# Kernel optimization log

Measured on AMD Instinct MI355X. Metric: run time of the kernel, lower is better.

## Reference

```python
import jax, jax.numpy as jnp
import numpy as np

DIM = 1024
HEADS = 16
HIDDEN = 4096
EPS = 1e-5

def setup_inputs() -> dict:
    key = jax.random.key(0)
    ks = jax.random.split(key, 8)
    s = 0.02
    return {
        "x": jax.random.normal(ks[0], (4, 1024, DIM), dtype=jnp.float32),
        "ln1_g": jnp.ones((DIM,), jnp.float32),
        "ln1_b": jnp.zeros((DIM,), jnp.float32),
        "w_qkv": jax.random.normal(ks[1], (DIM, 3 * DIM), jnp.float32) * s,
        "b_qkv": jnp.zeros((3 * DIM,), jnp.float32),
        "w_proj": jax.random.normal(ks[2], (DIM, DIM), jnp.float32) * s,
        "b_proj": jnp.zeros((DIM,), jnp.float32),
        "ln2_g": jnp.ones((DIM,), jnp.float32),
        "ln2_b": jnp.zeros((DIM,), jnp.float32),
        "w_fc1": jax.random.normal(ks[3], (DIM, HIDDEN), jnp.float32) * s,
        "b_fc1": jnp.zeros((HIDDEN,), jnp.float32),
        "w_fc2": jax.random.normal(ks[4], (HIDDEN, DIM), jnp.float32) * s,
        "b_fc2": jnp.zeros((DIM,), jnp.float32),
    }

def _layernorm(x, g, b):
    mu = jnp.mean(x, axis=-1, keepdims=True)
    var = jnp.mean(jnp.square(x - mu), axis=-1, keepdims=True)
    return (x - mu) * jax.lax.rsqrt(var + EPS) * g + b

def _block(x, ln1_g, ln1_b, w_qkv, b_qkv, w_proj, b_proj,
           ln2_g, ln2_b, w_fc1, b_fc1, w_fc2, b_fc2):
    B, N, C = x.shape
    H = HEADS
    Dh = C // H
    scale = Dh ** -0.5
    # --- attention branch (pre-norm) ---
    h = _layernorm(x, ln1_g, ln1_b)
    qkv = h @ w_qkv + b_qkv                       # [B,N,3C]
    qkv = qkv.reshape(B, N, 3, H, Dh)
    q, k, v = qkv[:, :, 0], qkv[:, :, 1], qkv[:, :, 2]  # [B,N,H,Dh]
    attn = jnp.einsum("bnhd,bmhd->bhnm", q, k) * scale  # [B,H,N,N]
    attn = jax.nn.softmax(attn, axis=-1)
    o = jnp.einsum("bhnm,bmhd->bnhd", attn, v).reshape(B, N, C)
    x = x + (o @ w_proj + b_proj)
    # --- MLP branch (pre-norm) ---
    h = _layernorm(x, ln2_g, ln2_b)
    h = jax.nn.gelu(h @ w_fc1 + b_fc1, approximate=False)
    x = x + (h @ w_fc2 + b_fc2)
    return x

def reference(x, ln1_g, ln1_b, w_qkv, b_qkv, w_proj, b_proj,
              ln2_g, ln2_b, w_fc1, b_fc1, w_fc2, b_fc2):
    return _block(x, ln1_g, ln1_b, w_qkv, b_qkv, w_proj, b_proj,
                  ln2_g, ln2_b, w_fc1, b_fc1, w_fc2, b_fc2)
```

## Files before the change

### kernel.cpp

```cpp
#include <hip/hip_runtime.h>
#include <hip/hip_bf16.h>

typedef __attribute__((ext_vector_type(8))) short bf16x8;
typedef __attribute__((ext_vector_type(4))) float f32x4;

__device__ __forceinline__ ushort f2bf(float f) {
  unsigned int u = __float_as_uint(f);
  u += 0x7fffu + ((u >> 16) & 1u);
  return (ushort)(u >> 16);
}

__device__ __forceinline__ void gl_lds16(const void* g, void* l) {
  __builtin_amdgcn_global_load_lds(
      (const __attribute__((address_space(1))) void*)g,
      (__attribute__((address_space(3))) void*)l, 16, 0, 0);
}

#define SB() __builtin_amdgcn_sched_barrier(0)

__global__ __launch_bounds__(256) void transpose_w(
    const float* __restrict__ W, ushort* __restrict__ Wt, int K, int N) {
  __shared__ float tile[32][33];
  const int tx = threadIdx.x, ty = threadIdx.y;
  const int bx = blockIdx.x, by = blockIdx.y;
#pragma unroll
  for (int j = 0; j < 4; j++)
    tile[ty + j * 8][tx] = W[(size_t)(by * 32 + ty + j * 8) * N + bx * 32 + tx];
  __syncthreads();
#pragma unroll
  for (int j = 0; j < 4; j++)
    Wt[(size_t)(bx * 32 + ty + j * 8) * K + by * 32 + tx] =
        f2bf(tile[tx][ty + j * 8]);
}

__global__ __launch_bounds__(256) void transpose_v(
    const ushort* __restrict__ qkv, ushort* __restrict__ vt) {
  __shared__ ushort tile[32][33];
  const int tx = threadIdx.x, ty = threadIdx.y;
  const int n0 = blockIdx.x * 32;
  const int d0 = blockIdx.y * 32;
  const int bh = blockIdx.z;
  const int bidx = bh >> 4, h = bh & 15;
#pragma unroll
  for (int j = 0; j < 4; j++)
    tile[ty + j * 8][tx] =
        qkv[(size_t)(bidx * 1024 + n0 + ty + j * 8) * 3072 + 2048 + h * 64 +
            d0 + tx];
  __syncthreads();
#pragma unroll
  for (int j = 0; j < 4; j++)
    vt[(size_t)(bh * 64 + d0 + ty + j * 8) * 1024 + n0 + tx] =
        tile[tx][ty + j * 8];
}

__global__ __launch_bounds__(256) void ln_bf16(
    const float* __restrict__ x, const float* __restrict__ g,
    const float* __restrict__ b, ushort* __restrict__ out) {
  const int row = blockIdx.x;
  const int t = threadIdx.x;
  float4 v = ((const float4*)(x + (size_t)row * 1024))[t];
  float s = v.x + v.y + v.z + v.w;
  float ss = v.x * v.x + v.y * v.y + v.z * v.z + v.w * v.w;
#pragma unroll
  for (int msk = 1; msk < 64; msk <<= 1) {
    s += __shfl_xor(s, msk);
    ss += __shfl_xor(ss, msk);
  }
  __shared__ float red[8];
  const int wv = t >> 6, ln = t & 63;
  if (ln == 0) { red[wv * 2] = s; red[wv * 2 + 1] = ss; }
  __syncthreads();
  s = red[0] + red[2] + red[4] + red[6];
  ss = red[1] + red[3] + red[5] + red[7];
  const float mu = s * (1.0f / 1024.0f);
  const float var = ss * (1.0f / 1024.0f) - mu * mu;
  const float rstd = rsqrtf(var + 1e-5f);
  float4 gv = ((const float4*)g)[t];
  float4 bv = ((const float4*)b)[t];
  ushort4 o;
  o.x = f2bf((v.x - mu) * rstd * gv.x + bv.x);
  o.y = f2bf((v.y - mu) * rstd * gv.y + bv.y);
  o.z = f2bf((v.z - mu) * rstd * gv.z + bv.z);
  o.w = f2bf((v.w - mu) * rstd * gv.w + bv.w);
  ((ushort4*)(out + (size_t)row * 1024))[t] = o;
}

template <int BM, int BN, int NW, int OCC, int EPI>
__global__ __launch_bounds__(NW * 64, OCC) void gemm32(
    const ushort* __restrict__ A, const ushort* __restrict__ Bt,
    const float* __restrict__ bias, const float* __restrict__ resid,
    void* __restrict__ outp, int M, int N, int K, int cw, int ch, int xw) {
  constexpr int WN = NW / 2;
  constexpr int BWN = BN / WN;
  constexpr int MF = BM / 2 / 16;
  constexpr int NF = BWN / 16;
  constexpr int CA = BM / 64, CB = BN / 64;
  __shared__ ushort smem[2 * (BM + BN) * 32];
  const int t = threadIdx.x;
  const int lane = t & 63, wid = t >> 6;
  const int lr = lane & 15, lc = lane >> 4;
  const int wr = wid / WN, wc = wid % WN;

  const int flat = blockIdx.y * gridDim.x + blockIdx.x;
  const int xcd = flat & 7, li = flat >> 3;
  const int bx = (xcd % xw) * cw + (li % cw);
  const int by = (xcd / xw) * ch + (li / cw);
  const int m0 = by * BM, n0 = bx * BN;
  const int nkt = K >> 5;

  const int uoff = ((t & 3) ^ ((t >> 3) & 3)) * 8;
  const int au = (lc ^ ((lr >> 1) & 3)) * 8;

  f32x4 acc[MF][NF];
#pragma unroll
  for (int m = 0; m < MF; m++)
#pragma unroll
    for (int n = 0; n < NF; n++) acc[m][n] = (f32x4){0.f, 0.f, 0.f, 0.f};

  auto stage = [&](int bb, int kt) {
#pragma unroll
    for (int c = 0; c < CA; c++)
      gl_lds16(A + (size_t)(m0 + c * 64 + (t >> 2)) * K + (size_t)(kt * 32) +
                   uoff,
               &smem[bb * BM * 32 + c * 2048 + wid * 512]);
#pragma unroll
    for (int c = 0; c < CB; c++)
      gl_lds16(Bt + (size_t)(n0 + c * 64 + (t >> 2)) * K + (size_t)(kt * 32) +
                   uoff,
               &smem[2 * BM * 32 + bb * BN * 32 + c * 2048 + wid * 512]);
  };
  auto rdA = [&](int bb, int mf) {
    return *(const bf16x8*)&smem[bb * BM * 32 +
                                 (wr * (BM / 2) + mf * 16 + lr) * 32 + au];
  };
  auto rdB = [&](int bb, int nf) {
    return *(const bf16x8*)&smem[2 * BM * 32 + bb * BN * 32 +
                                 (wc * BWN + nf * 16 + lr) * 32 + au];
  };

  stage(0, 0);
  asm volatile("s_waitcnt vmcnt(0)" ::: "memory");
  SB(); __builtin_amdgcn_s_barrier(); SB();

  int b = 0;
  for (int kt = 0; kt < nkt; kt++, b ^= 1) {
    if (kt + 1 < nkt) stage(b ^ 1, kt + 1);

    bf16x8 Br[NF];
#pragma unroll
    for (int nf = 0; nf < NF; nf++) Br[nf] = rdB(b, nf);
    bf16x8 Ar[MF];
#pragma unroll
    for (int mf = 0; mf < MF; mf++) Ar[mf] = rdA(b, mf);
    __builtin_amdgcn_s_setprio(1);
#pragma unroll
    for (int mf = 0; mf < MF; mf++)
#pragma unroll
      for (int nf = 0; nf < NF; nf++)
        acc[mf][nf] = __builtin_amdgcn_mfma_f32_16x16x32_bf16(
            Ar[mf], Br[nf], acc[mf][nf], 0, 0, 0);
    __builtin_amdgcn_s_setprio(0);

    asm volatile("s_waitcnt vmcnt(0)" ::: "memory");
    SB(); __builtin_amdgcn_s_barrier(); SB();
  }

#pragma unroll
  for (int mf = 0; mf < MF; mf++) {
#pragma unroll
    for (int nf = 0; nf < NF; nf++) {
      const int gr0 = m0 + wr * (BM / 2) + mf * 16 + lc * 4;
      const int gc = n0 + wc * BWN + nf * 16 + lr;
      const float bs = bias[gc];
#pragma unroll
      for (int r = 0; r < 4; r++) {
        const float v = acc[mf][nf][r] + bs;
        const int gr = gr0 + r;
        if (EPI == 0) {
          ((ushort*)outp)[(size_t)gr * N + gc] = f2bf(v);
        } else if (EPI == 1) {
          const float gg = 0.5f * v * (1.0f + erff(v * 0.70710678118654752f));
          ((ushort*)outp)[(size_t)gr * N + gc] = f2bf(gg);
        } else {
          ((float*)outp)[(size_t)gr * N + gc] =
              v + resid[(size_t)gr * N + gc];
        }
      }
    }
  }
}

template <int BM, int BN, int NW, int EPI>
__global__ __launch_bounds__(NW * 64, 2) void gemm64(
    const ushort* __restrict__ A, const ushort* __restrict__ Bt,
    const float* __restrict__ bias, const float* __restrict__ resid,
    void* __restrict__ outp, int M, int N, int K, int cw, int ch, int xw) {
  constexpr int T = NW * 64;
  constexpr int WN = NW / 2;
  constexpr int BWN = BN / WN;
  constexpr int MF = BM / 2 / 16;
  constexpr int NF = BWN / 16;
  constexpr int CA = BM / 64, CB = BN / 64;
  constexpr int REP = 512 / T;
  __shared__ ushort smem[2 * (BM + BN) * 64];
  const int t = threadIdx.x;
  const int lane = t & 63, wid = t >> 6;
  const int lr = lane & 15, lc = lane >> 4;
  const int wr = wid / WN, wc = wid % WN;

  const int flat = blockIdx.y * gridDim.x + blockIdx.x;
  const int xcd = flat & 7, li = flat >> 3;
  const int bx = (xcd % xw) * cw + (li % cw);
  const int by = (xcd / xw) * ch + (li / cw);
  const int m0 = by * BM, n0 = bx * BN;
  const int nkt = K >> 6;

  const int uoff = ((t & 7) ^ ((t >> 3) & 7)) * 8;
  const int sx = lr & 7;
  const int au0 = (lc ^ sx) * 8;
  const int au1 = ((lc | 4) ^ sx) * 8;

  f32x4 acc[MF][NF];
#pragma unroll
  for (int m = 0; m < MF; m++)
#pragma unroll
    for (int n = 0; n < NF; n++) acc[m][n] = (f32x4){0.f, 0.f, 0.f, 0.f};

  auto stage = [&](int bb, int kt) {
#pragma unroll
    for (int c = 0; c < CA; c++)
#pragma unroll
      for (int r = 0; r < REP; r++)
        gl_lds16(A + (size_t)(m0 + c * 64 + ((r * T + t) >> 3)) * K +
                     (size_t)(kt * 64) + uoff,
                 &smem[bb * BM * 64 + c * 4096 + (r * T + wid * 64) * 8]);
#pragma unroll
    for (int c = 0; c < CB; c++)
#pragma unroll
      for (int r = 0; r < REP; r++)
        gl_lds16(Bt + (size_t)(n0 + c * 64 + ((r * T + t) >> 3)) * K +
                     (size_t)(kt * 64) + uoff,
                 &smem[2 * BM * 64 + bb * BN * 64 + c * 4096 +
                       (r * T + wid * 64) * 8]);
  };
  auto rdA = [&](int bb, int mf, int kk) {
    return *(const bf16x8*)&smem[bb * BM * 64 +
                                 (wr * (BM / 2) + mf * 16 + lr) * 64 +
                                 (kk ? au1 : au0)];
  };
  auto rdB = [&](int bb, int nf, int kk) {
    return *(const bf16x8*)&smem[2 * BM * 64 + bb * BN * 64 +
                                 (wc * BWN + nf * 16 + lr) * 64 +
                                 (kk ? au1 : au0)];
  };

  stage(0, 0);
  asm volatile("s_waitcnt vmcnt(0)" ::: "memory");
  SB(); __builtin_amdgcn_s_barrier(); SB();

  int b = 0;
  for (int kt = 0; kt < nkt; kt++, b ^= 1) {
    if (kt + 1 < nkt) stage(b ^ 1, kt + 1);

    bf16x8 Br[NF][2];
#pragma unroll
    for (int nf = 0; nf < NF; nf++) {
      Br[nf][0] = rdB(b, nf, 0);
      Br[nf][1] = rdB(b, nf, 1);
    }
#pragma unroll
    for (int mh = 0; mh < MF / 4; mh++) {
      bf16x8 Ar[4][2];
#pragma unroll
      for (int mf = 0; mf < 4; mf++) {
        Ar[mf][0] = rdA(b, mh * 4 + mf, 0);
        Ar[mf][1] = rdA(b, mh * 4 + mf, 1);
      }
      __builtin_amdgcn_s_setprio(1);
#pragma unroll
      for (int mf = 0; mf < 4; mf++)
#pragma unroll
        for (int nf = 0; nf < NF; nf++) {
          acc[mh * 4 + mf][nf] = __builtin_amdgcn_mfma_f32_16x16x32_bf16(
              Ar[mf][0], Br[nf][0], acc[mh * 4 + mf][nf], 0, 0, 0);
          acc[mh * 4 + mf][nf] = __builtin_amdgcn_mfma_f32_16x16x32_bf16(
              Ar[mf][1], Br[nf][1], acc[mh * 4 + mf][nf], 0, 0, 0);
        }
      __builtin_amdgcn_s_setprio(0);
    }

    asm volatile("s_waitcnt vmcnt(0)" ::: "memory");
    SB(); __builtin_amdgcn_s_barrier(); SB();
  }

#pragma unroll
  for (int mf = 0; mf < MF; mf++) {
#pragma unroll
    for (int nf = 0; nf < NF; nf++) {
      const int gr0 = m0 + wr * (BM / 2) + mf * 16 + lc * 4;
      const int gc = n0 + wc * BWN + nf * 16 + lr;
      const float bs = bias[gc];
#pragma unroll
      for (int r = 0; r < 4; r++) {
        const float v = acc[mf][nf][r] + bs;
        const int gr = gr0 + r;
        if (EPI == 0) {
          ((ushort*)outp)[(size_t)gr * N + gc] = f2bf(v);
        } else if (EPI == 1) {
          const float gg = 0.5f * v * (1.0f + erff(v * 0.70710678118654752f));
          ((ushort*)outp)[(size_t)gr * N + gc] = f2bf(gg);
        } else {
          ((float*)outp)[(size_t)gr * N + gc] =
              v + resid[(size_t)gr * N + gc];
        }
      }
    }
  }
}

__global__ __launch_bounds__(256) void attn_kernel(
    const ushort* __restrict__ qkv, const ushort* __restrict__ vt,
    ushort* __restrict__ o_out) {
  __shared__ ushort sK[4096];
  __shared__ ushort sV[4096];
  __shared__ ushort sP[4 * 32 * 72];
  const int t = threadIdx.x;
  const int lane = t & 63, wid = t >> 6;
  const int lr = lane & 15, lc = lane >> 4;
  const int qb = blockIdx.x;
  const int bh = blockIdx.y;
  const int bidx = bh >> 4, h = bh & 15;
  const size_t base = (size_t)bidx * 1024 * 3072;
  const int q0w = qb * 128 + wid * 32;

  bf16x8 qf[2][2];
#pragma unroll
  for (int nf = 0; nf < 2; nf++)
#pragma unroll
    for (int kd = 0; kd < 2; kd++)
      qf[nf][kd] = *(const bf16x8*)&qkv[base +
          (size_t)(q0w + nf * 16 + lr) * 3072 + h * 64 + kd * 32 + lc * 8];

  f32x4 oacc[4][2];
#pragma unroll
  for (int mf = 0; mf < 4; mf++)
#pragma unroll
    for (int nf = 0; nf < 2; nf++) oacc[mf][nf] = (f32x4){0.f, 0.f, 0.f, 0.f};
  float m_r[2] = {-1e30f, -1e30f};
  float l_r[2] = {0.f, 0.f};

  const int srow = lane >> 2;
  const int scol = (lane & 3) * 8;
  ushort* pw = sP + wid * 2304;

  for (int kv0 = 0; kv0 < 1024; kv0 += 64) {
    __syncthreads();
#pragma unroll
    for (int s = 0; s < 2; s++) {
      gl_lds16(qkv + base + (size_t)(kv0 + wid * 16 + srow) * 3072 + 1024 +
                   h * 64 + s * 32 + scol,
               sK + s * 2048 + wid * 512);
      gl_lds16(vt + (size_t)(bh * 64 + wid * 16 + srow) * 1024 + kv0 + s * 32 +
                   scol,
               sV + s * 2048 + wid * 512);
    }
    __syncthreads();

    f32x4 st[4][2];
#pragma unroll
    for (int mf = 0; mf < 4; mf++) {
      bf16x8 ka0 = *(const bf16x8*)&sK[(mf * 16 + lr) * 32 + lc * 8];
      bf16x8 ka1 = *(const bf16x8*)&sK[2048 + (mf * 16 + lr) * 32 + lc * 8];
#pragma unroll
      for (int nf = 0; nf < 2; nf++) {
        f32x4 z = (f32x4){0.f, 0.f, 0.f, 0.f};
        z = __builtin_amdgcn_mfma_f32_16x16x32_bf16(ka0, qf[nf][0], z, 0, 0, 0);
        z = __builtin_amdgcn_mfma_f32_16x16x32_bf16(ka1, qf[nf][1], z, 0, 0, 0);
        st[mf][nf] = z;
      }
    }

#pragma unroll
    for (int nf = 0; nf < 2; nf++) {
      float mx = st[0][nf][0];
#pragma unroll
      for (int mf = 0; mf < 4; mf++)
        mx = fmaxf(mx, fmaxf(fmaxf(st[mf][nf][0], st[mf][nf][1]),
                             fmaxf(st[mf][nf][2], st[mf][nf][3])));
      mx = fmaxf(mx, __shfl_xor(mx, 16));
      mx = fmaxf(mx, __shfl_xor(mx, 32));
      mx *= 0.125f;
      const float mn = fmaxf(m_r[nf], mx);
      const float alpha = __expf(m_r[nf] - mn);
      m_r[nf] = mn;
      float rs = 0.f;
#pragma unroll
      for (int mf = 0; mf < 4; mf++) {
        const float p0 = __expf(fmaf(st[mf][nf][0], 0.125f, -mn));
        const float p1 = __expf(fmaf(st[mf][nf][1], 0.125f, -mn));
        const float p2 = __expf(fmaf(st[mf][nf][2], 0.125f, -mn));
        const float p3 = __expf(fmaf(st[mf][nf][3], 0.125f, -mn));
        rs += (p0 + p1) + (p2 + p3);
        uint2 u;
        u.x = (uint)f2bf(p0) | ((uint)f2bf(p1) << 16);
        u.y = (uint)f2bf(p2) | ((uint)f2bf(p3) << 16);
        *(uint2*)&pw[(nf * 16 + lr) * 72 + mf * 16 + lc * 4] = u;
      }
      rs += __shfl_xor(rs, 16);
      rs += __shfl_xor(rs, 32);
      l_r[nf] = l_r[nf] * alpha + rs;
#pragma unroll
      for (int mf = 0; mf < 4; mf++) {
        oacc[mf][nf][0] *= alpha;
        oacc[mf][nf][1] *= alpha;
        oacc[mf][nf][2] *= alpha;
        oacc[mf][nf][3] *= alpha;
      }
    }

#pragma unroll
    for (int ks = 0; ks < 2; ks++) {
      bf16x8 pb0 = *(const bf16x8*)&pw[lr * 72 + ks * 32 + lc * 8];
      bf16x8 pb1 = *(const bf16x8*)&pw[(16 + lr) * 72 + ks * 32 + lc * 8];
#pragma unroll
      for (int mf = 0; mf < 4; mf++) {
        bf16x8 va = *(const bf16x8*)&sV[ks * 2048 + (mf * 16 + lr) * 32 + lc * 8];
        oacc[mf][0] =
            __builtin_amdgcn_mfma_f32_16x16x32_bf16(va, pb0, oacc[mf][0], 0, 0, 0);
        oacc[mf][1] =
            __builtin_amdgcn_mfma_f32_16x16x32_bf16(va, pb1, oacc[mf][1], 0, 0, 0);
      }
    }
  }

  const float inv[2] = {1.f / l_r[0], 1.f / l_r[1]};
#pragma unroll
  for (int mf = 0; mf < 4; mf++)
#pragma unroll
    for (int nf = 0; nf < 2; nf++) {
      ushort4 o4;
      o4.x = f2bf(oacc[mf][nf][0] * inv[nf]);
      o4.y = f2bf(oacc[mf][nf][1] * inv[nf]);
      o4.z = f2bf(oacc[mf][nf][2] * inv[nf]);
      o4.w = f2bf(oacc[mf][nf][3] * inv[nf]);
      *(ushort4*)&o_out[(size_t)(bidx * 1024 + q0w + nf * 16 + lr) * 1024 +
                        h * 64 + mf * 16 + lc * 4] = o4;
    }
}

extern "C" void kernel_launch(void* const* d_in, const int* in_sizes, int n_in,
                              void* d_out, int out_size, void* d_ws,
                              size_t ws_size, hipStream_t stream) {
  const float* x      = (const float*)d_in[0];
  const float* ln1_g  = (const float*)d_in[1];
  const float* ln1_b  = (const float*)d_in[2];
  const float* w_qkv  = (const float*)d_in[3];
  const float* b_qkv  = (const float*)d_in[4];
  const float* w_proj = (const float*)d_in[5];
  const float* b_proj = (const float*)d_in[6];
  const float* ln2_g  = (const float*)d_in[7];
  const float* ln2_b  = (const float*)d_in[8];
  const float* w_fc1  = (const float*)d_in[9];
  const float* b_fc1  = (const float*)d_in[10];
  const float* w_fc2  = (const float*)d_in[11];
  const float* b_fc2  = (const float*)d_in[12];
  float* out = (float*)d_out;

  ushort* ws      = (ushort*)d_ws;
  ushort* wt_qkv  = ws;
  ushort* wt_proj = wt_qkv + 3072 * 1024;
  ushort* wt_fc1  = wt_proj + 1024 * 1024;
  ushort* wt_fc2  = wt_fc1 + 4096 * 1024;
  ushort* hbuf    = wt_fc2 + 1024 * 4096;
  ushort* qkv     = hbuf + 4096 * 1024;
  ushort* obuf    = qkv + 4096 * 3072;
  ushort* h3      = qkv;
  ushort* vtb     = hbuf;

  transpose_w<<<dim3(96, 32), dim3(32, 8), 0, stream>>>(w_qkv, wt_qkv, 1024, 3072);
  transpose_w<<<dim3(32, 32), dim3(32, 8), 0, stream>>>(w_proj, wt_proj, 1024, 1024);
  transpose_w<<<dim3(128, 32), dim3(32, 8), 0, stream>>>(w_fc1, wt_fc1, 1024, 4096);
  transpose_w<<<dim3(32, 128), dim3(32, 8), 0, stream>>>(w_fc2, wt_fc2, 4096, 1024);

  ln_bf16<<<4096, 256, 0, stream>>>(x, ln1_g, ln1_b, hbuf);
  gemm32<128, 128, 4, 4, 0><<<dim3(24, 32), 256, 0, stream>>>(
      hbuf, wt_qkv, b_qkv, nullptr, qkv, 4096, 3072, 1024, 12, 8, 2);
  transpose_v<<<dim3(32, 2, 64), dim3(32, 8), 0, stream>>>(qkv, vtb);
  attn_kernel<<<dim3(8, 64), 256, 0, stream>>>(qkv, vtb, obuf);
  gemm64<128, 64, 4, 2><<<dim3(16, 32), 256, 0, stream>>>(
      obuf, wt_proj, b_proj, x, out, 4096, 1024, 1024, 8, 8, 2);
  ln_bf16<<<4096, 256, 0, stream>>>(out, ln2_g, ln2_b, hbuf);
  gemm32<128, 128, 4, 4, 1><<<dim3(32, 32), 256, 0, stream>>>(
      hbuf, wt_fc1, b_fc1, nullptr, h3, 4096, 4096, 1024, 16, 8, 2);
  gemm64<128, 64, 4, 2><<<dim3(16, 32), 256, 0, stream>>>(
      h3, wt_fc2, b_fc2, out, out, 4096, 1024, 4096, 8, 8, 2);
}
```

Baseline: 229.3 us.

## Replace 128x128 gemm32 with 512-thread triple-buffered 256-row tile GEMM for QKV and FC1

The QKV and FC1 GEMMs move to a new kernel with 8 waves, 256-row tiles (192 or 256 columns) and a three-stage LDS ring that prefetches two K-steps ahead and waits with partial vmcnt instead of draining all loads. Larger tiles raise operand reuse per LDS byte, and the deeper pipeline is meant to hide global-load latency. The A fragments are loaded in two halves to limit register pressure. In exchange the grid shrinks to 256 blocks with more LDS and registers per block, and vmcnt(4) is hardcoded, which assumes a particular per-stage load count.

```diff
diff --git a/kernel.cpp b/kernel.cpp
--- a/kernel.cpp
+++ b/kernel.cpp
@@ -85,21 +85,21 @@
   ((ushort4*)(out + (size_t)row * 1024))[t] = o;
 }
 
-template <int BM, int BN, int NW, int OCC, int EPI>
-__global__ __launch_bounds__(NW * 64, OCC) void gemm32(
+template <int BM, int BN, int EPI>
+__global__ __launch_bounds__(512, 2) void gemmr3(
     const ushort* __restrict__ A, const ushort* __restrict__ Bt,
-    const float* __restrict__ bias, const float* __restrict__ resid,
-    void* __restrict__ outp, int M, int N, int K, int cw, int ch, int xw) {
-  constexpr int WN = NW / 2;
-  constexpr int BWN = BN / WN;
-  constexpr int MF = BM / 2 / 16;
+    const float* __restrict__ bias, void* __restrict__ outp,
+    int M, int N, int K, int cw, int ch, int xw) {
+  constexpr int T = 512;
+  constexpr int BWN = BN / 4;
+  constexpr int MF = 8;
   constexpr int NF = BWN / 16;
-  constexpr int CA = BM / 64, CB = BN / 64;
-  __shared__ ushort smem[2 * (BM + BN) * 32];
+  constexpr int ASLOT = BM * 4, BSLOT = BN * 4;
+  __shared__ ushort smem[3 * (BM + BN) * 32];
   const int t = threadIdx.x;
   const int lane = t & 63, wid = t >> 6;
   const int lr = lane & 15, lc = lane >> 4;
-  const int wr = wid / WN, wc = wid % WN;
+  const int wr = wid >> 2, wc = wid & 3;
 
   const int flat = blockIdx.y * gridDim.x + blockIdx.x;
   const int xcd = flat & 7, li = flat >> 3;
@@ -108,7 +108,6 @@
   const int m0 = by * BM, n0 = bx * BN;
   const int nkt = K >> 5;
 
-  const int uoff = ((t & 3) ^ ((t >> 3) & 3)) * 8;
   const int au = (lc ^ ((lr >> 1) & 3)) * 8;
 
   f32x4 acc[MF][NF];
@@ -119,57 +118,74 @@
 
   auto stage = [&](int bb, int kt) {
 #pragma unroll
-    for (int c = 0; c < CA; c++)
-      gl_lds16(A + (size_t)(m0 + c * 64 + (t >> 2)) * K + (size_t)(kt * 32) +
-                   uoff,
-               &smem[bb * BM * 32 + c * 2048 + wid * 512]);
-#pragma unroll
-    for (int c = 0; c < CB; c++)
-      gl_lds16(Bt + (size_t)(n0 + c * 64 + (t >> 2)) * K + (size_t)(kt * 32) +
-                   uoff,
-               &smem[2 * BM * 32 + bb * BN * 32 + c * 2048 + wid * 512]);
+    for (int s0 = 0; s0 < ASLOT; s0 += T) {
+      const int s = s0 + t;
+      gl_lds16(A + (size_t)(m0 + (s >> 2)) * K + (size_t)(kt * 32) +
+                   ((s & 3) ^ ((s >> 3) & 3)) * 8,
+               &smem[bb * BM * 32 + s * 8]);
+    }
+#pragma unroll
+    for (int s0 = 0; s0 < BSLOT; s0 += T) {
+      const int rem = BSLOT - s0;
+      const int s = s0 + (rem >= T ? t : (t & (rem - 1)));
+      gl_lds16(Bt + (size_t)(n0 + (s >> 2)) * K + (size_t)(kt * 32) +
+                   ((s & 3) ^ ((s >> 3) & 3)) * 8,
+               &smem[3 * BM * 32 + bb * BN * 32 + s * 8]);
+    }
   };
   auto rdA = [&](int bb, int mf) {
-    return *(const bf16x8*)&smem[bb * BM * 32 +
-                                 (wr * (BM / 2) + mf * 16 + lr) * 32 + au];
+    return *(const bf16x8*)&smem[bb * BM * 32 + (wr * 128 + mf * 16 + lr) * 32 +
+                                 au];
   };
   auto rdB = [&](int bb, int nf) {
-    return *(const bf16x8*)&smem[2 * BM * 32 + bb * BN * 32 +
+    return *(const bf16x8*)&smem[3 * BM * 32 + bb * BN * 32 +
                                  (wc * BWN + nf * 16 + lr) * 32 + au];
   };
 
   stage(0, 0);
-  asm volatile("s_waitcnt vmcnt(0)" ::: "memory");
+  if (nkt > 1) {
+    stage(1, 1);
+    asm volatile("s_waitcnt vmcnt(4)" ::: "memory");
+  } else {
+    asm volatile("s_waitcnt vmcnt(0)" ::: "memory");
+  }
   SB(); __builtin_amdgcn_s_barrier(); SB();
 
-  int b = 0;
-  for (int kt = 0; kt < nkt; kt++, b ^= 1) {
-    if (kt + 1 < nkt) stage(b ^ 1, kt + 1);
+  int rb = 0;
+  for (int kt = 0; kt < nkt; kt++) {
+    const int sb = (rb >= 1) ? rb - 1 : 2;
+    const bool pf = (kt + 2 < nkt);
+    if (pf) stage(sb, kt + 2);
 
     bf16x8 Br[NF];
 #pragma unroll
-    for (int nf = 0; nf < NF; nf++) Br[nf] = rdB(b, nf);
-    bf16x8 Ar[MF];
-#pragma unroll
-    for (int mf = 0; mf < MF; mf++) Ar[mf] = rdA(b, mf);
-    __builtin_amdgcn_s_setprio(1);
-#pragma unroll
-    for (int mf = 0; mf < MF; mf++)
-#pragma unroll
-      for (int nf = 0; nf < NF; nf++)
-        acc[mf][nf] = __builtin_amdgcn_mfma_f32_16x16x32_bf16(
-            Ar[mf], Br[nf], acc[mf][nf], 0, 0, 0);
-    __builtin_amdgcn_s_setprio(0);
-
-    asm volatile("s_waitcnt vmcnt(0)" ::: "memory");
+    for (int nf = 0; nf < NF; nf++) Br[nf] = rdB(rb, nf);
+#pragma unroll
+    for (int mh = 0; mh < 2; mh++) {
+      bf16x8 Ar[4];
+#pragma unroll
+      for (int mf = 0; mf < 4; mf++) Ar[mf] = rdA(rb, mh * 4 + mf);
+      __builtin_amdgcn_s_setprio(1);
+#pragma unroll
+      for (int mf = 0; mf < 4; mf++)
+#pragma unroll
+        for (int nf = 0; nf < NF; nf++)
+          acc[mh * 4 + mf][nf] = __builtin_amdgcn_mfma_f32_16x16x32_bf16(
+              Ar[mf], Br[nf], acc[mh * 4 + mf][nf], 0, 0, 0);
+      __builtin_amdgcn_s_setprio(0);
+    }
+
+    if (pf) asm volatile("s_waitcnt vmcnt(4)" ::: "memory");
+    else    asm volatile("s_waitcnt vmcnt(0)" ::: "memory");
     SB(); __builtin_amdgcn_s_barrier(); SB();
+    rb = (rb == 2) ? 0 : rb + 1;
   }
 
 #pragma unroll
   for (int mf = 0; mf < MF; mf++) {
 #pragma unroll
     for (int nf = 0; nf < NF; nf++) {
-      const int gr0 = m0 + wr * (BM / 2) + mf * 16 + lc * 4;
+      const int gr0 = m0 + wr * 128 + mf * 16 + lc * 4;
       const int gc = n0 + wc * BWN + nf * 16 + lr;
       const float bs = bias[gc];
 #pragma unroll
@@ -178,12 +194,9 @@
         const int gr = gr0 + r;
         if (EPI == 0) {
           ((ushort*)outp)[(size_t)gr * N + gc] = f2bf(v);
-        } else if (EPI == 1) {
+        } else {
           const float gg = 0.5f * v * (1.0f + erff(v * 0.70710678118654752f));
           ((ushort*)outp)[(size_t)gr * N + gc] = f2bf(gg);
-        } else {
-          ((float*)outp)[(size_t)gr * N + gc] =
-              v + resid[(size_t)gr * N + gc];
         }
       }
     }
@@ -483,15 +496,15 @@
   transpose_w<<<dim3(32, 128), dim3(32, 8), 0, stream>>>(w_fc2, wt_fc2, 4096, 1024);
 
   ln_bf16<<<4096, 256, 0, stream>>>(x, ln1_g, ln1_b, hbuf);
-  gemm32<128, 128, 4, 4, 0><<<dim3(24, 32), 256, 0, stream>>>(
-      hbuf, wt_qkv, b_qkv, nullptr, qkv, 4096, 3072, 1024, 12, 8, 2);
+  gemmr3<256, 192, 0><<<dim3(16, 16), 512, 0, stream>>>(
+      hbuf, wt_qkv, b_qkv, qkv, 4096, 3072, 1024, 4, 8, 4);
   transpose_v<<<dim3(32, 2, 64), dim3(32, 8), 0, stream>>>(qkv, vtb);
   attn_kernel<<<dim3(8, 64), 256, 0, stream>>>(qkv, vtb, obuf);
   gemm64<128, 64, 4, 2><<<dim3(16, 32), 256, 0, stream>>>(
       obuf, wt_proj, b_proj, x, out, 4096, 1024, 1024, 8, 8, 2);
   ln_bf16<<<4096, 256, 0, stream>>>(out, ln2_g, ln2_b, hbuf);
-  gemm32<128, 128, 4, 4, 1><<<dim3(32, 32), 256, 0, stream>>>(
-      hbuf, wt_fc1, b_fc1, nullptr, h3, 4096, 4096, 1024, 16, 8, 2);
+  gemmr3<256, 256, 1><<<dim3(16, 16), 512, 0, stream>>>(
+      hbuf, wt_fc1, b_fc1, h3, 4096, 4096, 1024, 4, 8, 4);
   gemm64<128, 64, 4, 2><<<dim3(16, 32), 256, 0, stream>>>(
       h3, wt_fc2, b_fc2, out, out, 4096, 1024, 4096, 8, 8, 2);
 }
```

New measurement: 240.1 us. 1.05x slower.
